# Optimization experiments

Measured on AMD Instinct MI355X. Metric: run time of the kernel, lower is better.

Reference implementation:

```python
import jax, jax.numpy as jnp
import numpy as np

MOVING_RATE = 0.999

def _l2norm(x, eps=1e-12):
    # matches F.normalize(dim=-1): x / max(||x||, eps)
    return x / jnp.maximum(jnp.linalg.norm(x, axis=-1, keepdims=True), eps)

def setup_inputs() -> dict:
    k = jax.random.key(0)
    k1, k2, k3 = jax.random.split(k, 3)
    B, S, K, D = 8192, 14, 512, 256
    return {
        "key": jax.random.normal(k1, (B, S, D), dtype=jnp.float32),
        "value": jax.random.normal(k2, (B, S, D), dtype=jnp.float32),
        "memory": jax.random.normal(k3, (S, K, D), dtype=jnp.float32),
    }

def reference(key, value, memory):
    # key, value: (B, S, D); memory: (S, K, D). update=True path, all slots batched.
    K = memory.shape[1]
    xn = _l2norm(key)                                   # (B,S,D)
    mn = _l2norm(memory)                                # (S,K,D)
    score = jnp.einsum('bsd,skd->bsk', xn, mn)          # (B,S,K)

    # --- EMA codebook update (value is detached in the original) ---
    v = jax.lax.stop_gradient(value)
    ind = jnp.argmax(score, axis=-1)                    # (B,S)
    oh = jax.nn.one_hot(ind, K, dtype=value.dtype)      # (B,S,K)
    oh_sum = oh.sum(axis=0)                             # (S,K)
    emb_sum = jnp.einsum('bsd,bsk->skd', v, oh)         # (S,K,D)
    emb_mean = emb_sum / (oh_sum[..., None] + 1e-6)
    new_mem = memory * MOVING_RATE + emb_mean * (1.0 - MOVING_RATE)

    # --- re-score against updated codebook ---
    score2 = jnp.einsum('bsd,skd->bsk', xn, _l2norm(new_mem))
    ind2 = jnp.argmax(score2, axis=-1)
    oh2 = jax.nn.one_hot(ind2, K, dtype=value.dtype)    # (B,S,K)

    # note: original adds value[:, 0, :] (slot 0) for EVERY slot i — kept faithfully
    out = value[:, :1, :] + jnp.einsum('bsk,skd->bsd', oh2, new_mem)  # (B,S,D)
    return out, new_mem
```

## Files before the change

kernel.cpp:

```cpp
#include <hip/hip_runtime.h>
#include <cstddef>
#include <cstdint>

#define B_ 8192
#define S_ 14
#define K_ 512
#define D_ 256

typedef __attribute__((ext_vector_type(8))) short bfx8;
typedef __attribute__((ext_vector_type(4))) float fx4;

typedef __attribute__((address_space(3))) unsigned int       lds_u32;
typedef const __attribute__((address_space(1))) unsigned int glb_u32;

__device__ __forceinline__ void gload16(const void* g, void* l) {
    __builtin_amdgcn_global_load_lds((glb_u32*)g, (lds_u32*)l, 16, 0, 0);
}

__device__ __forceinline__ unsigned short f2bf(float x) {
    union { float f; unsigned int u; } v; v.f = x;
    unsigned int r = (v.u + 0x7FFFu + ((v.u >> 16) & 1u)) >> 16;
    return (unsigned short)r;
}
__device__ __forceinline__ float bf2f(unsigned short h) {
    union { unsigned int u; float f; } v; v.u = ((unsigned int)h) << 16;
    return v.f;
}

__global__ __launch_bounds__(64) void rownorm_kernel(
    const float* __restrict__ rows, float* __restrict__ invn)
{
    const int row  = blockIdx.x;
    const int lane = threadIdx.x;
    const float4 v = *reinterpret_cast<const float4*>(rows + (size_t)row * D_ + lane * 4);
    float ss = v.x * v.x + v.y * v.y + v.z * v.z + v.w * v.w;
    #pragma unroll
    for (int m = 32; m >= 1; m >>= 1) ss += __shfl_xor(ss, m, 64);
    if (lane == 0) invn[row] = 1.0f / fmaxf(sqrtf(ss), 1e-12f);
}

__global__ __launch_bounds__(256) void split_key_kernel(
    const float* __restrict__ key,
    unsigned short* __restrict__ ph, unsigned short* __restrict__ pm,
    unsigned short* __restrict__ pl)
{
    const int gid  = blockIdx.x * 256 + threadIdx.x;
    const int e    = gid * 4;
    const int b    = e / (S_ * D_);
    const int rem  = e - b * (S_ * D_);
    const int s    = rem >> 8;
    const int d    = rem & 255;
    const float4 x = *reinterpret_cast<const float4*>(key + e);
    const size_t o = ((size_t)s * B_ + b) * D_ + d;

    float xs[4] = { x.x, x.y, x.z, x.w };
    unsigned short hh[4], mm[4], ll[4];
    #pragma unroll
    for (int i = 0; i < 4; ++i) {
        unsigned short a = f2bf(xs[i]);
        float r1 = xs[i] - bf2f(a);
        unsigned short bq = f2bf(r1);
        float r2 = r1 - bf2f(bq);
        unsigned short c = f2bf(r2);
        hh[i] = a; mm[i] = bq; ll[i] = c;
    }
    *reinterpret_cast<ushort4*>(ph + o) = make_ushort4(hh[0], hh[1], hh[2], hh[3]);
    *reinterpret_cast<ushort4*>(pm + o) = make_ushort4(mm[0], mm[1], mm[2], mm[3]);
    *reinterpret_cast<ushort4*>(pl + o) = make_ushort4(ll[0], ll[1], ll[2], ll[3]);
}

__global__ __launch_bounds__(64) void splitnorm_mem_kernel(
    const float* __restrict__ mem,
    unsigned short* __restrict__ ph, unsigned short* __restrict__ pm,
    unsigned short* __restrict__ pl, float* __restrict__ invn)
{
    const int row  = blockIdx.x;
    const int lane = threadIdx.x;
    const size_t e = (size_t)row * D_ + lane * 4;
    const float4 x = *reinterpret_cast<const float4*>(mem + e);

    float xs[4] = { x.x, x.y, x.z, x.w };
    unsigned short hh[4], mm[4], ll[4];
    #pragma unroll
    for (int i = 0; i < 4; ++i) {
        unsigned short a = f2bf(xs[i]);
        float r1 = xs[i] - bf2f(a);
        unsigned short bq = f2bf(r1);
        float r2 = r1 - bf2f(bq);
        unsigned short c = f2bf(r2);
        hh[i] = a; mm[i] = bq; ll[i] = c;
    }
    *reinterpret_cast<ushort4*>(ph + e) = make_ushort4(hh[0], hh[1], hh[2], hh[3]);
    *reinterpret_cast<ushort4*>(pm + e) = make_ushort4(mm[0], mm[1], mm[2], mm[3]);
    *reinterpret_cast<ushort4*>(pl + e) = make_ushort4(ll[0], ll[1], ll[2], ll[3]);

    float ss = x.x * x.x + x.y * x.y + x.z * x.z + x.w * x.w;
    #pragma unroll
    for (int m = 32; m >= 1; m >>= 1) ss += __shfl_xor(ss, m, 64);
    if (lane == 0) invn[row] = 1.0f / fmaxf(sqrtf(ss), 1e-12f);
}

__global__ __launch_bounds__(512, 4) void gemm_argmax_kernel(
    const unsigned short* __restrict__ kh, const unsigned short* __restrict__ km,
    const unsigned short* __restrict__ kl,
    const unsigned short* __restrict__ mh, const unsigned short* __restrict__ mm_,
    const unsigned short* __restrict__ ml,
    const float* __restrict__ invn,
    float* __restrict__ pV, int* __restrict__ pI)
{
    __shared__ __align__(16) short T[36864];

    const int orig = blockIdx.x;
    const int wg   = (orig & 7) * 224 + (orig >> 3);
    const int by   = wg & 3;
    const int bx   = (wg >> 2) & 31;
    const int s    = wg >> 7;

    const int t    = threadIdx.x;
    const int b0   = bx * 256;
    const int n0   = by * 128;
    const int w    = t >> 6;
    const int lane = t & 63;
    const int wm   = w >> 1;
    const int wn   = w & 1;
    const int lr   = lane & 15, lg = lane >> 4;

    const size_t sB = (size_t)s * B_;
    const size_t sK = (size_t)s * K_;

    const unsigned short* __restrict__ APl[3] = { kh, km, kl };
    const unsigned short* __restrict__ BPl[3] = { mh, mm_, ml };

    fx4 acc[4][4];
    #pragma unroll
    for (int i = 0; i < 4; ++i)
        #pragma unroll
        for (int j = 0; j < 4; ++j) acc[i][j] = (fx4)0.0f;

    const int rsub = lane >> 2;
    const int csw  = (((lane & 3) ^ ((lane >> 3) & 3)) * 8);
    const int rdof = ((lg ^ ((lr >> 1) & 3)) * 8);

    for (int dc = 0; dc < 8; ++dc) {
        const int dco = dc * 32 + csw;
        #pragma unroll
        for (int p = 0; p < 3; ++p) {
            #pragma unroll
            for (int u = 0; u < 2; ++u) {
                const int R0 = w * 32 + u * 16;
                gload16(APl[p] + (sB + b0 + R0 + rsub) * D_ + dco,
                        &T[p * 8192 + R0 * 32]);
            }
            {
                const int R0 = w * 16;
                gload16(BPl[p] + (sK + n0 + R0 + rsub) * D_ + dco,
                        &T[24576 + p * 4096 + R0 * 32]);
            }
        }
        __syncthreads();

        #pragma unroll
        for (int ap = 0; ap < 3; ++ap) {
            bfx8 af[4];
            #pragma unroll
            for (int i = 0; i < 4; ++i)
                af[i] = *reinterpret_cast<const bfx8*>(
                    &T[ap * 8192 + (wm * 64 + i * 16 + lr) * 32 + rdof]);
            #pragma unroll
            for (int bp = 0; bp < 3 - ap; ++bp) {
                bfx8 bfr[4];
                #pragma unroll
                for (int j = 0; j < 4; ++j)
                    bfr[j] = *reinterpret_cast<const bfx8*>(
                        &T[24576 + bp * 4096 + (wn * 64 + j * 16 + lr) * 32 + rdof]);
                __builtin_amdgcn_s_setprio(1);
                #pragma unroll
                for (int i = 0; i < 4; ++i)
                    #pragma unroll
                    for (int j = 0; j < 4; ++j)
                        acc[i][j] = __builtin_amdgcn_mfma_f32_16x16x32_bf16(
                            af[i], bfr[j], acc[i][j], 0, 0, 0);
                __builtin_amdgcn_s_setprio(0);
            }
        }
        __syncthreads();
    }

    float* sInv = reinterpret_cast<float*>(&T[0]);
    float* bVp  = sInv + 128;
    int*   bIp  = reinterpret_cast<int*>(bVp + 512);

    if (t < 128) sInv[t] = invn[sK + n0 + t];
    __syncthreads();

    #pragma unroll
    for (int i = 0; i < 4; ++i) {
        #pragma unroll
        for (int r = 0; r < 4; ++r) {
            float bv = -3.4e38f; int bi = 0x7fffffff;
            #pragma unroll
            for (int j = 0; j < 4; ++j) {
                const int kloc = wn * 64 + j * 16 + lr;
                const float v  = acc[i][j][r] * sInv[kloc];
                const int  kg  = n0 + kloc;
                if (v > bv || (v == bv && kg < bi)) { bv = v; bi = kg; }
            }
            #pragma unroll
            for (int msk = 1; msk < 16; msk <<= 1) {
                const float ov = __shfl_xor(bv, msk, 64);
                const int   oi = __shfl_xor(bi, msk, 64);
                if (ov > bv || (ov == bv && oi < bi)) { bv = ov; bi = oi; }
            }
            if (lr == 0) {
                const int mrow = wm * 64 + i * 16 + lg * 4 + r;
                bVp[mrow * 2 + wn] = bv; bIp[mrow * 2 + wn] = bi;
            }
        }
    }
    __syncthreads();

    if (t < 256) {
        const float v0 = bVp[t * 2], v1 = bVp[t * 2 + 1];
        const int   i0 = bIp[t * 2], i1 = bIp[t * 2 + 1];
        const bool take1 = (v1 > v0) || (v1 == v0 && i1 < i0);
        const size_t o = ((size_t)s * 4 + by) * B_ + b0 + t;
        pV[o] = take1 ? v1 : v0;
        pI[o] = take1 ? i1 : i0;
    }
}

__global__ __launch_bounds__(256) void combine1_kernel(
    const float* __restrict__ pV, const int* __restrict__ pI,
    int* __restrict__ ind1)
{
    const int idx = blockIdx.x * 256 + threadIdx.x;
    const int s   = idx >> 13;
    const int b   = idx & 8191;
    float bv = -3.4e38f; int bi = 0x7fffffff;
    #pragma unroll
    for (int nb = 0; nb < 4; ++nb) {
        const size_t o = ((size_t)s * 4 + nb) * B_ + b;
        const float v = pV[o]; const int i = pI[o];
        if (v > bv || (v == bv && i < bi)) { bv = v; bi = i; }
    }
    ind1[idx] = bi;
}

__global__ __launch_bounds__(256) void combine2_out_kernel(
    const float* __restrict__ pV, const int* __restrict__ pI,
    const float* __restrict__ value, const float* __restrict__ newmem,
    float* __restrict__ out)
{
    const int row  = blockIdx.x * 4 + (threadIdx.x >> 6);
    const int lane = threadIdx.x & 63;
    const int s    = row >> 13;
    const int b    = row & 8191;
    float bv = -3.4e38f; int bi = 0x7fffffff;
    #pragma unroll
    for (int nb = 0; nb < 4; ++nb) {
        const size_t o = ((size_t)s * 4 + nb) * B_ + b;
        const float v = pV[o]; const int i = pI[o];
        if (v > bv || (v == bv && i < bi)) { bv = v; bi = i; }
    }
    const float4 vv = *reinterpret_cast<const float4*>(
        value + (size_t)b * (S_ * D_) + lane * 4);
    const float4 mmv = *reinterpret_cast<const float4*>(
        newmem + ((size_t)s * K_ + bi) * D_ + lane * 4);
    float4 o4;
    o4.x = vv.x + mmv.x; o4.y = vv.y + mmv.y;
    o4.z = vv.z + mmv.z; o4.w = vv.w + mmv.w;
    *reinterpret_cast<float4*>(out + ((size_t)b * S_ + s) * D_ + lane * 4) = o4;
}

__global__ __launch_bounds__(256) void u1_hist_kernel(
    const int* __restrict__ ind1, int* __restrict__ hist)
{
    __shared__ int h[K_];
    const int t = threadIdx.x, c = blockIdx.x, s = blockIdx.y;
    h[t] = 0; h[t + 256] = 0;
    __syncthreads();
    const int k = ind1[(size_t)s * B_ + c * 256 + t];
    atomicAdd(&h[k], 1);
    __syncthreads();
    hist[((size_t)s * 32 + c) * K_ + t]       = h[t];
    hist[((size_t)s * 32 + c) * K_ + t + 256] = h[t + 256];
}

__global__ __launch_bounds__(512) void u2_scan_kernel(
    int* __restrict__ hist, int* __restrict__ cnt, int* __restrict__ offs)
{
    __shared__ int sc[K_];
    const int k = threadIdx.x, s = blockIdx.x;
    int run = 0;
    for (int c = 0; c < 32; ++c) {
        const size_t o = ((size_t)s * 32 + c) * K_ + k;
        const int x = hist[o];
        hist[o] = run;
        run += x;
    }
    cnt[s * K_ + k] = run;
    sc[k] = run;
    __syncthreads();
    for (int off = 1; off < K_; off <<= 1) {
        int v = (k >= off) ? sc[k - off] : 0;
        __syncthreads();
        sc[k] += v;
        __syncthreads();
    }
    offs[s * K_ + k] = sc[k] - run;
}

__global__ __launch_bounds__(256) void u3_scatter_kernel(
    const int* __restrict__ ind1, const int* __restrict__ hist,
    const int* __restrict__ offs, int* __restrict__ csr)
{
    __shared__ int sk[256];
    const int t = threadIdx.x, c = blockIdx.x, s = blockIdx.y;
    const int b = c * 256 + t;
    const int k = ind1[(size_t)s * B_ + b];
    sk[t] = k;
    __syncthreads();
    int rank = 0;
    for (int j = 0; j < t; ++j) rank += (sk[j] == k);
    const int pos = offs[s * K_ + k] + hist[((size_t)s * 32 + c) * K_ + k] + rank;
    csr[(size_t)s * B_ + pos] = b;
}

__global__ __launch_bounds__(64) void u4_gather_kernel(
    const int* __restrict__ csr, const int* __restrict__ cnt,
    const int* __restrict__ offs, const float* __restrict__ value,
    const float* __restrict__ memory, float* __restrict__ newmem)
{
    const int k = blockIdx.x, s = blockIdx.y, lane = threadIdx.x;
    const int n = cnt[s * K_ + k];
    const int base = offs[s * K_ + k];
    float4 a; a.x = a.y = a.z = a.w = 0.0f;
    for (int i = 0; i < n; ++i) {
        const int b = csr[(size_t)s * B_ + base + i];
        const float4 v = *reinterpret_cast<const float4*>(
            value + ((size_t)b * S_ + s) * D_ + lane * 4);
        a.x += v.x; a.y += v.y; a.z += v.z; a.w += v.w;
    }
    const float inv = 1.0f / ((float)n + 1e-6f);
    const size_t o = ((size_t)s * K_ + k) * D_ + lane * 4;
    const float4 mo = *reinterpret_cast<const float4*>(memory + o);
    float4 r;
    r.x = mo.x * 0.999f + a.x * inv * 0.001f;
    r.y = mo.y * 0.999f + a.y * inv * 0.001f;
    r.z = mo.z * 0.999f + a.z * inv * 0.001f;
    r.w = mo.w * 0.999f + a.w * inv * 0.001f;
    *reinterpret_cast<float4*>(newmem + o) = r;
}

template <int MODE>
__global__ __launch_bounds__(256) void score_argmax_kernel(
    const float* __restrict__ key, const float* __restrict__ mem,
    const float* __restrict__ invn, const float* __restrict__ value,
    float* __restrict__ out, int* __restrict__ ind_out)
{
    __shared__ __align__(16) float kt[64][36];
    __shared__ __align__(16) float mt[64][36];
    __shared__ float redV[64][16];
    __shared__ int   redI[64][16];

    const int t  = threadIdx.x;
    const int s  = blockIdx.y;
    const int b0 = blockIdx.x * 64;
    const int tb = t & 15;
    const int tk = t >> 4;

    float best[4]; int bidx[4];
    #pragma unroll
    for (int i = 0; i < 4; ++i) { best[i] = -3.4e38f; bidx[i] = 0; }

    for (int kc = 0; kc < 8; ++kc) {
        float acc[4][4];
        #pragma unroll
        for (int i = 0; i < 4; ++i)
            #pragma unroll
            for (int j = 0; j < 4; ++j) acc[i][j] = 0.0f;

        for (int dc = 0; dc < 8; ++dc) {
            #pragma unroll
            for (int u = 0; u < 2; ++u) {
                const int f = t + u * 256;
                const int row = f >> 3;
                const int c4 = f & 7;
                *reinterpret_cast<float4*>(&kt[row][c4 * 4]) =
                    *reinterpret_cast<const float4*>(
                        key + (((size_t)(b0 + row)) * S_ + s) * D_ + dc * 32 + c4 * 4);
                *reinterpret_cast<float4*>(&mt[row][c4 * 4]) =
                    *reinterpret_cast<const float4*>(
                        mem + (((size_t)s * K_) + kc * 64 + row) * D_ + dc * 32 + c4 * 4);
            }
            __syncthreads();
            #pragma unroll
            for (int d4 = 0; d4 < 8; ++d4) {
                float4 a[4], b[4];
                #pragma unroll
                for (int i = 0; i < 4; ++i)
                    a[i] = *reinterpret_cast<const float4*>(&kt[tb + i * 16][d4 * 4]);
                #pragma unroll
                for (int j = 0; j < 4; ++j)
                    b[j] = *reinterpret_cast<const float4*>(&mt[tk + j * 16][d4 * 4]);
                #pragma unroll
                for (int i = 0; i < 4; ++i)
                    #pragma unroll
                    for (int j = 0; j < 4; ++j)
                        acc[i][j] += a[i].x * b[j].x + a[i].y * b[j].y +
                                     a[i].z * b[j].z + a[i].w * b[j].w;
            }
            __syncthreads();
        }
        #pragma unroll
        for (int j = 0; j < 4; ++j) {
            const int kabs = kc * 64 + tk + j * 16;
            const float inv = invn[s * K_ + kabs];
            #pragma unroll
            for (int i = 0; i < 4; ++i) {
                const float v = acc[i][j] * inv;
                if (v > best[i] || (v == best[i] && kabs < bidx[i])) {
                    best[i] = v; bidx[i] = kabs;
                }
            }
        }
    }
    #pragma unroll
    for (int i = 0; i < 4; ++i) {
        redV[tb + i * 16][tk] = best[i];
        redI[tb + i * 16][tk] = bidx[i];
    }
    __syncthreads();
    if (t < 64) {
        float bv = redV[t][0]; int bi = redI[t][0];
        #pragma unroll
        for (int g = 1; g < 16; ++g) {
            const float v = redV[t][g]; const int ix = redI[t][g];
            if (v > bv || (v == bv && ix < bi)) { bv = v; bi = ix; }
        }
        if (MODE == 0) ind_out[(size_t)s * B_ + b0 + t] = bi;
        else           redI[t][0] = bi;
    }
    if (MODE == 1) {
        __syncthreads();
        const int w = t >> 6, lane = t & 63;
        for (int r = w; r < 64; r += 4) {
            const int bg = b0 + r;
            const int kk = redI[r][0];
            const float4 vv = *reinterpret_cast<const float4*>(
                value + (size_t)bg * (S_ * D_) + lane * 4);
            const float4 mmv = *reinterpret_cast<const float4*>(
                mem + ((size_t)s * K_ + kk) * D_ + lane * 4);
            float4 o;
            o.x = vv.x + mmv.x; o.y = vv.y + mmv.y;
            o.z = vv.z + mmv.z; o.w = vv.w + mmv.w;
            *reinterpret_cast<float4*>(
                out + (((size_t)bg) * S_ + s) * D_ + lane * 4) = o;
        }
    }
}

__global__ __launch_bounds__(256) void update_kernel(
    const int* __restrict__ ind1, const float* __restrict__ value,
    const float* __restrict__ memory, float* __restrict__ newmem)
{
    const int k0 = blockIdx.x * 4, s = blockIdx.y, t = threadIdx.x;
    __shared__ int sIdx[256];
    float a0 = 0.f, a1 = 0.f, a2 = 0.f, a3 = 0.f;
    int c0 = 0, c1 = 0, c2 = 0, c3 = 0;
    for (int b0 = 0; b0 < B_; b0 += 256) {
        sIdx[t] = ind1[(size_t)s * B_ + b0 + t];
        __syncthreads();
        for (int bb = 0; bb < 256; ++bb) {
            const int ix = sIdx[bb];
            const unsigned r = (unsigned)(ix - k0);
            if (r < 4u) {
                const float v = value[(((size_t)(b0 + bb)) * S_ + s) * D_ + t];
                if      (r == 0u) { a0 += v; ++c0; }
                else if (r == 1u) { a1 += v; ++c1; }
                else if (r == 2u) { a2 += v; ++c2; }
                else              { a3 += v; ++c3; }
            }
        }
        __syncthreads();
    }
    const float accs[4] = { a0, a1, a2, a3 };
    const int   cns [4] = { c0, c1, c2, c3 };
    #pragma unroll
    for (int kk = 0; kk < 4; ++kk) {
        const size_t off = ((size_t)s * K_ + k0 + kk) * D_ + t;
        const float mean = accs[kk] / ((float)cns[kk] + 1e-6f);
        newmem[off] = memory[off] * 0.999f + mean * 0.001f;
    }
}

extern "C" void kernel_launch(void* const* d_in, const int* in_sizes, int n_in,
                              void* d_out, int out_size, void* d_ws, size_t ws_size,
                              hipStream_t stream)
{
    const float* key    = (const float*)d_in[0];
    const float* value  = (const float*)d_in[1];
    const float* memory = (const float*)d_in[2];

    float* out    = (float*)d_out;
    float* newmem = out + (size_t)B_ * S_ * D_;

    const size_t keyPlane = (size_t)S_ * B_ * D_;
    const size_t memPlane = (size_t)S_ * K_ * D_;
    char* p = (char*)d_ws;
    size_t need = 0;
    auto alloc = [&](size_t bytes) -> char* {
        char* r = p + need;
        need += (bytes + 255) & ~(size_t)255;
        return r;
    };
    unsigned short* kh  = (unsigned short*)alloc(keyPlane * 2);
    unsigned short* km  = (unsigned short*)alloc(keyPlane * 2);
    unsigned short* kl  = (unsigned short*)alloc(keyPlane * 2);
    unsigned short* mh  = (unsigned short*)alloc(memPlane * 2);
    unsigned short* mm  = (unsigned short*)alloc(memPlane * 2);
    unsigned short* ml  = (unsigned short*)alloc(memPlane * 2);
    float* invn   = (float*)alloc((size_t)S_ * K_ * 4);
    float* pV     = (float*)alloc((size_t)S_ * 4 * B_ * 4);
    int*   pI     = (int*)  alloc((size_t)S_ * 4 * B_ * 4);
    int*   ind1   = (int*)  alloc((size_t)S_ * B_ * 4);
    int*   hist   = (int*)  alloc((size_t)S_ * 32 * K_ * 4);
    int*   cnt    = (int*)  alloc((size_t)S_ * K_ * 4);
    int*   offs   = (int*)  alloc((size_t)S_ * K_ * 4);
    int*   csr    = (int*)  alloc((size_t)S_ * B_ * 4);

    if (ws_size >= need) {
        split_key_kernel<<<dim3((B_ * S_ * D_) / 1024), 256, 0, stream>>>(key, kh, km, kl);
        splitnorm_mem_kernel<<<dim3(S_ * K_), 64, 0, stream>>>(memory, mh, mm, ml, invn);

        gemm_argmax_kernel<<<dim3(1792), 512, 0, stream>>>(
            kh, km, kl, mh, mm, ml, invn, pV, pI);
        combine1_kernel<<<dim3((S_ * B_) / 256), 256, 0, stream>>>(pV, pI, ind1);

        u1_hist_kernel<<<dim3(32, S_), 256, 0, stream>>>(ind1, hist);
        u2_scan_kernel<<<dim3(S_), 512, 0, stream>>>(hist, cnt, offs);
        u3_scatter_kernel<<<dim3(32, S_), 256, 0, stream>>>(ind1, hist, offs, csr);
        u4_gather_kernel<<<dim3(K_, S_), 64, 0, stream>>>(csr, cnt, offs, value, memory, newmem);

        splitnorm_mem_kernel<<<dim3(S_ * K_), 64, 0, stream>>>(newmem, mh, mm, ml, invn);

        gemm_argmax_kernel<<<dim3(1792), 512, 0, stream>>>(
            kh, km, kl, mh, mm, ml, invn, pV, pI);
        combine2_out_kernel<<<dim3((S_ * B_) / 4), 256, 0, stream>>>(
            pV, pI, value, newmem, out);
    } else {
        float* invn1 = (float*)d_ws;
        float* invn2 = invn1 + S_ * K_;
        int*   find1 = (int*)(invn2 + S_ * K_);

        rownorm_kernel<<<dim3(S_ * K_), 64, 0, stream>>>(memory, invn1);
        score_argmax_kernel<0><<<dim3(B_ / 64, S_), 256, 0, stream>>>(
            key, memory, invn1, nullptr, nullptr, find1);
        update_kernel<<<dim3(K_ / 4, S_), 256, 0, stream>>>(find1, value, memory, newmem);
        rownorm_kernel<<<dim3(S_ * K_), 64, 0, stream>>>(newmem, invn2);
        score_argmax_kernel<1><<<dim3(B_ / 64, S_), 256, 0, stream>>>(
            key, newmem, invn2, value, out, nullptr);
    }
}
```

Measured before the change: 459.3 us.

## Double-buffer A tiles in LDS, read B fragments directly from global

Reshapes the GEMM-argmax tile from 256x128 to 128x256 per block, using 2x4 waves and halving the number of N-partials. The A (key) tiles are now double-buffered in LDS so the next chunk's loads overlap the current MFMAs. B (memory codebook) fragments are loaded straight from global/cache instead of being staged through LDS. This removes one sync per iteration and cuts LDS use, which may raise occupancy, but the direct B loads add global-memory latency inside the MFMA loop. The combine kernels are updated to reduce over two partials instead of four.

```diff
diff --git a/kernel.cpp b/kernel.cpp
--- a/kernel.cpp
+++ b/kernel.cpp
@@ -108,28 +108,30 @@
     const float* __restrict__ invn,
     float* __restrict__ pV, int* __restrict__ pI)
 {
-    __shared__ __align__(16) short T[36864];
+    __shared__ __align__(16) short T[2][12288];
 
     const int orig = blockIdx.x;
     const int wg   = (orig & 7) * 224 + (orig >> 3);
-    const int by   = wg & 3;
-    const int bx   = (wg >> 2) & 31;
+    const int by   = wg & 1;
+    const int bx   = (wg >> 1) & 63;
     const int s    = wg >> 7;
 
     const int t    = threadIdx.x;
-    const int b0   = bx * 256;
-    const int n0   = by * 128;
+    const int b0   = bx * 128;
+    const int n0   = by * 256;
     const int w    = t >> 6;
     const int lane = t & 63;
-    const int wm   = w >> 1;
-    const int wn   = w & 1;
+    const int wm   = w >> 2;
+    const int wn   = w & 3;
     const int lr   = lane & 15, lg = lane >> 4;
 
     const size_t sB = (size_t)s * B_;
     const size_t sK = (size_t)s * K_;
 
     const unsigned short* __restrict__ APl[3] = { kh, km, kl };
-    const unsigned short* __restrict__ BPl[3] = { mh, mm_, ml };
+
+    const size_t bRow = (sK + n0 + wn * 64 + lr) * (size_t)D_ + lg * 8;
+    const unsigned short* __restrict__ BB[3] = { mh + bRow, mm_ + bRow, ml + bRow };
 
     fx4 acc[4][4];
     #pragma unroll
@@ -141,23 +143,22 @@
     const int csw  = (((lane & 3) ^ ((lane >> 3) & 3)) * 8);
     const int rdof = ((lg ^ ((lr >> 1) & 3)) * 8);
 
+    auto stage = [&](int nb, int dcv) {
+        const int dco = dcv * 32 + csw;
+        const int R0  = w * 16;
+        #pragma unroll
+        for (int p = 0; p < 3; ++p)
+            gload16(APl[p] + (sB + b0 + R0 + rsub) * D_ + dco,
+                    &T[nb][p * 4096 + R0 * 32]);
+    };
+
+    stage(0, 0);
+    __syncthreads();
+
     for (int dc = 0; dc < 8; ++dc) {
-        const int dco = dc * 32 + csw;
-        #pragma unroll
-        for (int p = 0; p < 3; ++p) {
-            #pragma unroll
-            for (int u = 0; u < 2; ++u) {
-                const int R0 = w * 32 + u * 16;
-                gload16(APl[p] + (sB + b0 + R0 + rsub) * D_ + dco,
-                        &T[p * 8192 + R0 * 32]);
-            }
-            {
-                const int R0 = w * 16;
-                gload16(BPl[p] + (sK + n0 + R0 + rsub) * D_ + dco,
-                        &T[24576 + p * 4096 + R0 * 32]);
-            }
-        }
-        __syncthreads();
+        if (dc < 7) stage((dc + 1) & 1, dc + 1);
+        const short* Tb = &T[dc & 1][0];
+        const int dcd = dc * 32;
 
         #pragma unroll
         for (int ap = 0; ap < 3; ++ap) {
@@ -165,14 +166,14 @@
             #pragma unroll
             for (int i = 0; i < 4; ++i)
                 af[i] = *reinterpret_cast<const bfx8*>(
-                    &T[ap * 8192 + (wm * 64 + i * 16 + lr) * 32 + rdof]);
+                    &Tb[ap * 4096 + (wm * 64 + i * 16 + lr) * 32 + rdof]);
             #pragma unroll
             for (int bp = 0; bp < 3 - ap; ++bp) {
                 bfx8 bfr[4];
                 #pragma unroll
                 for (int j = 0; j < 4; ++j)
                     bfr[j] = *reinterpret_cast<const bfx8*>(
-                        &T[24576 + bp * 4096 + (wn * 64 + j * 16 + lr) * 32 + rdof]);
+                        BB[bp] + (size_t)j * 16 * D_ + dcd);
                 __builtin_amdgcn_s_setprio(1);
                 #pragma unroll
                 for (int i = 0; i < 4; ++i)
@@ -186,11 +187,11 @@
         __syncthreads();
     }
 
-    float* sInv = reinterpret_cast<float*>(&T[0]);
-    float* bVp  = sInv + 128;
+    float* sInv = reinterpret_cast<float*>(&T[0][0]);
+    float* bVp  = sInv + 256;
     int*   bIp  = reinterpret_cast<int*>(bVp + 512);
 
-    if (t < 128) sInv[t] = invn[sK + n0 + t];
+    if (t < 256) sInv[t] = invn[sK + n0 + t];
     __syncthreads();
 
     #pragma unroll
@@ -213,19 +214,22 @@
             }
             if (lr == 0) {
                 const int mrow = wm * 64 + i * 16 + lg * 4 + r;
-                bVp[mrow * 2 + wn] = bv; bIp[mrow * 2 + wn] = bi;
-            }
-        }
-    }
-    __syncthreads();
-
-    if (t < 256) {
-        const float v0 = bVp[t * 2], v1 = bVp[t * 2 + 1];
-        const int   i0 = bIp[t * 2], i1 = bIp[t * 2 + 1];
-        const bool take1 = (v1 > v0) || (v1 == v0 && i1 < i0);
-        const size_t o = ((size_t)s * 4 + by) * B_ + b0 + t;
-        pV[o] = take1 ? v1 : v0;
-        pI[o] = take1 ? i1 : i0;
+                bVp[mrow * 4 + wn] = bv; bIp[mrow * 4 + wn] = bi;
+            }
+        }
+    }
+    __syncthreads();
+
+    if (t < 128) {
+        float bv = bVp[t * 4]; int bi = bIp[t * 4];
+        #pragma unroll
+        for (int g = 1; g < 4; ++g) {
+            const float v = bVp[t * 4 + g]; const int ix = bIp[t * 4 + g];
+            if (v > bv || (v == bv && ix < bi)) { bv = v; bi = ix; }
+        }
+        const size_t o = ((size_t)s * 2 + by) * B_ + b0 + t;
+        pV[o] = bv;
+        pI[o] = bi;
     }
 }
 
@@ -238,8 +242,8 @@
     const int b   = idx & 8191;
     float bv = -3.4e38f; int bi = 0x7fffffff;
     #pragma unroll
-    for (int nb = 0; nb < 4; ++nb) {
-        const size_t o = ((size_t)s * 4 + nb) * B_ + b;
+    for (int nb = 0; nb < 2; ++nb) {
+        const size_t o = ((size_t)s * 2 + nb) * B_ + b;
         const float v = pV[o]; const int i = pI[o];
         if (v > bv || (v == bv && i < bi)) { bv = v; bi = i; }
     }
@@ -257,8 +261,8 @@
     const int b    = row & 8191;
     float bv = -3.4e38f; int bi = 0x7fffffff;
     #pragma unroll
-    for (int nb = 0; nb < 4; ++nb) {
-        const size_t o = ((size_t)s * 4 + nb) * B_ + b;
+    for (int nb = 0; nb < 2; ++nb) {
+        const size_t o = ((size_t)s * 2 + nb) * B_ + b;
         const float v = pV[o]; const int i = pI[o];
         if (v > bv || (v == bv && i < bi)) { bv = v; bi = i; }
     }
```

After: 902.3 us. 96.5% more time.

## Double-buffer LDS tiles to overlap global loads with MFMA in score GEMM

Applied to the files above, without the earlier changes.

Splits the LDS tile into two buffers and prefetches the next D-chunk with async global-to-LDS loads while the current chunk is consumed by MFMAs, using explicit vmcnt waits and raw barriers. It also hoists all B-fragment LDS reads for the three split planes ahead of the A loop. The aim is to hide global load latency behind compute. In exchange LDS use doubles to about 144KB per block and launch bounds drop occupancy from 4 to 2, and the extra fragment registers raise register pressure.

```diff
diff --git a/kernel.cpp b/kernel.cpp
--- a/kernel.cpp
+++ b/kernel.cpp
@@ -100,7 +100,7 @@
     if (lane == 0) invn[row] = 1.0f / fmaxf(sqrtf(ss), 1e-12f);
 }
 
-__global__ __launch_bounds__(512, 4) void gemm_argmax_kernel(
+__global__ __launch_bounds__(512, 2) void gemm_argmax_kernel(
     const unsigned short* __restrict__ kh, const unsigned short* __restrict__ km,
     const unsigned short* __restrict__ kl,
     const unsigned short* __restrict__ mh, const unsigned short* __restrict__ mm_,
@@ -108,7 +108,7 @@
     const float* __restrict__ invn,
     float* __restrict__ pV, int* __restrict__ pI)
 {
-    __shared__ __align__(16) short T[36864];
+    __shared__ __align__(16) short T[2][36864];
 
     const int orig = blockIdx.x;
     const int wg   = (orig & 7) * 224 + (orig >> 3);
@@ -141,23 +141,45 @@
     const int csw  = (((lane & 3) ^ ((lane >> 3) & 3)) * 8);
     const int rdof = ((lg ^ ((lr >> 1) & 3)) * 8);
 
-    for (int dc = 0; dc < 8; ++dc) {
-        const int dco = dc * 32 + csw;
+    auto stage = [&](int nb, int dcv) {
+        const int dco = dcv * 32 + csw;
         #pragma unroll
         for (int p = 0; p < 3; ++p) {
             #pragma unroll
             for (int u = 0; u < 2; ++u) {
                 const int R0 = w * 32 + u * 16;
                 gload16(APl[p] + (sB + b0 + R0 + rsub) * D_ + dco,
-                        &T[p * 8192 + R0 * 32]);
+                        &T[nb][p * 8192 + R0 * 32]);
             }
             {
                 const int R0 = w * 16;
                 gload16(BPl[p] + (sK + n0 + R0 + rsub) * D_ + dco,
-                        &T[24576 + p * 4096 + R0 * 32]);
-            }
-        }
-        __syncthreads();
+                        &T[nb][24576 + p * 4096 + R0 * 32]);
+            }
+        }
+    };
+
+    stage(0, 0);
+
+    for (int dc = 0; dc < 8; ++dc) {
+        if (dc < 7) {
+            stage((dc + 1) & 1, dc + 1);
+            asm volatile("s_waitcnt vmcnt(9)" ::: "memory");
+        } else {
+            asm volatile("s_waitcnt vmcnt(0)" ::: "memory");
+        }
+        asm volatile("s_barrier" ::: "memory");
+        __builtin_amdgcn_sched_barrier(0);
+
+        const short* Tb = &T[dc & 1][0];
+
+        bfx8 bf[3][4];
+        #pragma unroll
+        for (int bp = 0; bp < 3; ++bp)
+            #pragma unroll
+            for (int j = 0; j < 4; ++j)
+                bf[bp][j] = *reinterpret_cast<const bfx8*>(
+                    &Tb[24576 + bp * 4096 + (wn * 64 + j * 16 + lr) * 32 + rdof]);
 
         #pragma unroll
         for (int ap = 0; ap < 3; ++ap) {
@@ -165,28 +187,25 @@
             #pragma unroll
             for (int i = 0; i < 4; ++i)
                 af[i] = *reinterpret_cast<const bfx8*>(
-                    &T[ap * 8192 + (wm * 64 + i * 16 + lr) * 32 + rdof]);
+                    &Tb[ap * 8192 + (wm * 64 + i * 16 + lr) * 32 + rdof]);
             #pragma unroll
             for (int bp = 0; bp < 3 - ap; ++bp) {
-                bfx8 bfr[4];
-                #pragma unroll
-                for (int j = 0; j < 4; ++j)
-                    bfr[j] = *reinterpret_cast<const bfx8*>(
-                        &T[24576 + bp * 4096 + (wn * 64 + j * 16 + lr) * 32 + rdof]);
                 __builtin_amdgcn_s_setprio(1);
                 #pragma unroll
                 for (int i = 0; i < 4; ++i)
                     #pragma unroll
                     for (int j = 0; j < 4; ++j)
                         acc[i][j] = __builtin_amdgcn_mfma_f32_16x16x32_bf16(
-                            af[i], bfr[j], acc[i][j], 0, 0, 0);
+                            af[i], bf[bp][j], acc[i][j], 0, 0, 0);
                 __builtin_amdgcn_s_setprio(0);
             }
         }
-        __syncthreads();
-    }
-
-    float* sInv = reinterpret_cast<float*>(&T[0]);
+
+        __builtin_amdgcn_sched_barrier(0);
+        asm volatile("s_barrier" ::: "memory");
+    }
+
+    float* sInv = reinterpret_cast<float*>(&T[0][0]);
     float* bVp  = sInv + 128;
     int*   bIp  = reinterpret_cast<int*>(bVp + 512);
 
```

New measurement: 572.4 us. +24.6%, slower.
